# Performance work log

Measured on AMD Instinct MI355X. Metric: run time of the kernel, lower is better.

## Reference

```python
import jax, jax.numpy as jnp
import numpy as np

DT = 1e-3  # integration timestep (init kwarg dt)


def setup_inputs() -> dict:
    key = jax.random.key(0)
    ks = jax.random.split(key, 10)
    B, T, S, H = 4096, 2048, 1, 64
    # physically sensible signals: v ~ N(0,1), 0 < F_c < F_s so g > 0
    v = jax.random.normal(ks[0], (B, T, S), dtype=jnp.float32)
    F_c = 0.5 + jax.random.uniform(ks[1], (B, T, S), dtype=jnp.float32)
    F_s = F_c + 0.5 + 0.5 * jax.random.uniform(ks[2], (B, T, S), dtype=jnp.float32)
    x = jnp.concatenate([v, F_c, F_s], axis=-1)  # [B, T, 3*S]
    u01 = lambda k, shp: jax.random.uniform(k, shp, minval=0.0, maxval=0.1, dtype=jnp.float32)
    return {
        "x": x,
        "sigma_1": u01(ks[3], (1, S)),
        "sigma_2": u01(ks[4], (1, S)),
        "alpha": u01(ks[5], (1, S)),
        "v_s": u01(ks[6], (1, S)),
        "W1": jax.random.normal(ks[7], (2 * S, H), dtype=jnp.float32) * 0.1,
        "b1": jnp.zeros((H,), jnp.float32),
        "W2": jax.random.normal(ks[8], (H, S), dtype=jnp.float32) * 0.1,
        "b2": jnp.zeros((S,), jnp.float32),
    }


def reference(x, sigma_1, sigma_2, alpha, v_s, W1, b1, W2, b2):
    """LuGreCell.callv3 unrolled over time via lax.scan. x: [B,T,3S] -> F: [B,T,S]."""
    s1 = jnp.abs(sigma_1)
    s2 = jnp.abs(sigma_2)

    def step(sz0, xt):  # sz0: [B,S], xt: [B,3S]
        v, F_c, F_s = jnp.split(xt, 3, axis=-1)
        # sigma_call: MLP on concat([v, sz_0])
        mi = jnp.concatenate([v, sz0], axis=-1)  # [B, 2S]
        sigma_0 = jax.nn.softplus(jnp.tanh(mi @ W1 + b1) @ W2 + b2)  # [B, S]
        g = F_c + (F_s - F_c) * jnp.exp(-jnp.abs(v / v_s) ** alpha)
        k = g * jnp.sign(v)
        sz = k + (sz0 - k) * jnp.exp(-DT * sigma_0 * jnp.abs(v) / g)
        zdot = v - sz * jnp.abs(v) / g  # uses pre-clip sz, as in original
        sz = jnp.clip(sz, -F_s, F_s)
        F = sz + s1 * zdot + s2 * v
        return sz, F

    B = x.shape[0]
    S = x.shape[-1] // 3
    xT = jnp.swapaxes(x, 0, 1)  # [T, B, 3S]
    sz_init = jnp.zeros((B, S), x.dtype)
    _, F_seq = jax.lax.scan(step, sz_init, xT)  # F_seq: [T, B, S]
    return jnp.swapaxes(F_seq, 0, 1)  # [B, T, S]
```

## Files before the change

### kernel.cpp

```cpp
#include <hip/hip_runtime.h>


#define DT 1e-3f
#define NV 256
#define VMINF (-6.6f)
#define VMAXF (6.6f)
#define ZAF   (2.56f)

__global__ __launch_bounds__(320) void coef_nodes_kernel(
    const float* __restrict__ W1,
    const float* __restrict__ b1,
    const float* __restrict__ W2,
    const float* __restrict__ b2,
    float* __restrict__ fbuf)
{
    const int iv = blockIdx.x;
    const int j  = threadIdx.x >> 6;
    const int h  = threadIdx.x & 63;
    const float v = VMINF + iv * ((VMAXF - VMINF) / (NV - 1));
    const float pn = 0.95105651629f * ZAF;
    const float qn = 0.58778525229f * ZAF;
    const float szv = (j == 0) ? pn : (j == 1) ? -pn
                    : (j == 2) ? qn : (j == 3) ? -qn : 0.f;
    const float pre = fmaf(v, W1[h], fmaf(szv, W1[64 + h], b1[h]));
    float c = W2[h] * tanhf(pre);
#pragma unroll
    for (int o = 32; o; o >>= 1) c += __shfl_down(c, o);
    if (h == 0) {
        const float y = c + b2[0];
        fbuf[iv * 5 + j] = fmaxf(y, 0.f) + log1pf(expf(-fabsf(y)));
    }
}

__global__ __launch_bounds__(256) void lugre_kernel(
    const float* __restrict__ x,
    const float* __restrict__ sigma1,
    const float* __restrict__ sigma2,
    const float* __restrict__ alpha_p,
    const float* __restrict__ vs_p,
    const float* __restrict__ fbuf,
    float* __restrict__ out,
    int B, int T)
{
    __shared__ float4 sA[NV];
    __shared__ float  sB[NV];
    __shared__ __align__(16) float preBuf[2][16][17][12];

    {
        const int iv = threadIdx.x;
        const float f0 = fbuf[iv * 5 + 0], f1 = fbuf[iv * 5 + 1];
        const float f2 = fbuf[iv * 5 + 2], f3 = fbuf[iv * 5 + 3];
        const float f4 = fbuf[iv * 5 + 4];
        const float pn = 0.95105651629f * ZAF;
        const float qn = 0.58778525229f * ZAF;
        const float P = pn * pn, Q = qn * qn;
        const float c0 = f4;
        const float ep = 0.5f * (f0 + f1) - c0;
        const float eq = 0.5f * (f2 + f3) - c0;
        const float op = 0.5f * (f0 - f1);
        const float oq = 0.5f * (f2 - f3);
        const float invPQ = 1.f / (P - Q);
        const float c4 = (ep / P - eq / Q) * invPQ;
        const float c2 = ep / P - c4 * P;
        const float c3 = (op / pn - oq / qn) * invPQ;
        const float c1 = op / pn - c3 * P;
        sA[iv] = make_float4(-DT * c0, -DT * c1, -DT * c2, -DT * c3);
        sB[iv] = -DT * c4;
    }

    const int lane16 = threadIdx.x & 15;
    const int grp    = threadIdx.x >> 4;
    const int b      = blockIdx.x * 16 + grp;
    const int NB     = T / 16;

    const float LOG2E = 1.4426950408889634f;
    const float s1v    = fabsf(sigma1[0]);
    const float s2v    = fabsf(sigma2[0]);
    const float s12    = s1v + s2v;
    const float alpha  = alpha_p[0];
    const float inv_vs = 1.0f / vs_p[0];
    const float SVC    = (NV - 1) / (VMAXF - VMINF);
    const float VOFF   = -VMINF * SVC;
    const float IMAX   = 254.999f;

    const float* __restrict__ xb = x + (size_t)b * T * 3;
    float* __restrict__ outb = out + (size_t)b * T;

    float sz = 0.f, Fkeep = 0.f;
    float xc0, xc1, xc2, xn0, xn1, xn2;

    auto mkpre_store = [&](float v, float fc, float fs, int WB) {
        const float av = fabsf(v);
        const float u  = av * inv_vs;
        const float lg = __builtin_amdgcn_logf(u);
        const float pw = __builtin_amdgcn_exp2f(alpha * lg);
        const float w_ = __builtin_amdgcn_exp2f(-LOG2E * pw);
        const float g  = fmaf(fs - fc, w_, fc);
        const float k  = copysignf(g, v);
        const float avg = av * __builtin_amdgcn_rcpf(g);
        const float fvr = __builtin_amdgcn_fmed3f(fmaf(v, SVC, VOFF), 0.f, IMAX);
        const float fvf = floorf(fvr);
        const float fr  = fvr - fvf;
        const int   iv  = (int)fvf;
        const float4 A0 = sA[iv], A1 = sA[iv + 1];
        const float  B0 = sB[iv], B1 = sB[iv + 1];
        float* wp = &preBuf[WB][grp][lane16][0];
        *(float4*)(wp + 0) = make_float4(fmaf(fr, A1.x - A0.x, A0.x),
                                         fmaf(fr, A1.y - A0.y, A0.y),
                                         fmaf(fr, A1.z - A0.z, A0.z),
                                         fmaf(fr, A1.w - A0.w, A0.w));
        *(float4*)(wp + 4) = make_float4(fmaf(fr, B1 - B0, B0), avg, k, -(s1v * avg));
        *(float4*)(wp + 8) = make_float4(s12 * v, fs, -fs, 0.f);
    };

    auto iter = [&](int n, int RB, int WB) {
        const float* rp = &preBuf[RB][grp][0][0];
        float4 s0a = *(const float4*)(rp + 0);
        float4 s0b = *(const float4*)(rp + 4);
        float4 s0c = *(const float4*)(rp + 8);
        float4 s1a = *(const float4*)(rp + 12);
        float4 s1b = *(const float4*)(rp + 16);
        float4 s1c = *(const float4*)(rp + 20);
        const int bl = min(n + 3, NB - 1);
        const int tl = 3 * (16 * bl + lane16);
        const float f0 = xb[tl], f1 = xb[tl + 1], f2 = xb[tl + 2];
        mkpre_store(xc0, xc1, xc2, WB);

#pragma unroll
        for (int t = 0; t < 16; ++t) {
            float4 na = s1a, nb = s1b, nc = s1c;
            if (t < 14) {
                const float* q = rp + (t + 2) * 12;
                na = *(const float4*)(q + 0);
                nb = *(const float4*)(q + 4);
                nc = *(const float4*)(q + 8);
            }
            const float h   = fmaf(fmaf(fmaf(fmaf(s0b.x, sz, s0a.w), sz, s0a.z), sz, s0a.y), sz, s0a.x);
            const float xd  = h * s0b.y;
            const float dd  = fmaf(xd, fmaf(xd, 0.5f, 1.f), 1.f);
            const float szn = fmaf(dd, sz - s0b.z, s0b.z);
            const float szc = __builtin_amdgcn_fmed3f(szn, s0c.z, s0c.y);
            const float F   = fmaf(s0b.w, szn, s0c.x + szc);
            sz = szc;
            Fkeep = (lane16 == t) ? F : Fkeep;
            s0a = s1a; s0b = s1b; s0c = s1c;
            s1a = na;  s1b = nb;  s1c = nc;
        }
        outb[16 * n + lane16] = Fkeep;
        xc0 = xn0; xc1 = xn1; xc2 = xn2;
        xn0 = f0;  xn1 = f1;  xn2 = f2;
    };

    const int t0i = 3 * lane16;
    const float p0 = xb[t0i], p1 = xb[t0i + 1], p2 = xb[t0i + 2];
    const int t1i = 3 * (16 + lane16);
    xc0 = xb[t1i]; xc1 = xb[t1i + 1]; xc2 = xb[t1i + 2];
    const int t2i = 3 * (32 + lane16);
    xn0 = xb[t2i]; xn1 = xb[t2i + 1]; xn2 = xb[t2i + 2];

    __syncthreads();
    mkpre_store(p0, p1, p2, 0);

    for (int nn = 0; nn < NB; nn += 2) {
        iter(nn, 0, 1);
        iter(nn + 1, 1, 0);
    }
}

extern "C" void kernel_launch(void* const* d_in, const int* in_sizes, int n_in,
                              void* d_out, int out_size, void* d_ws, size_t ws_size,
                              hipStream_t stream) {
    const float* x  = (const float*)d_in[0];
    const float* s1 = (const float*)d_in[1];
    const float* s2 = (const float*)d_in[2];
    const float* al = (const float*)d_in[3];
    const float* vs = (const float*)d_in[4];
    const float* W1 = (const float*)d_in[5];
    const float* b1 = (const float*)d_in[6];
    const float* W2 = (const float*)d_in[7];
    const float* b2 = (const float*)d_in[8];
    float* out  = (float*)d_out;
    float* fbuf = (float*)d_ws;

    const int T = 2048;
    const int B = out_size / T;

    coef_nodes_kernel<<<NV, 320, 0, stream>>>(W1, b1, W2, b2, fbuf);
    lugre_kernel<<<B / 16, 256, 0, stream>>>(x, s1, s2, al, vs, fbuf, out, B, T);
}
```

Before: 264.8 us.

## Shorten serial recurrence chain, shrink per-step buffer, move coefficient table to global

Coefficient fitting moves into the node kernel, which writes final polynomial tables to global memory. The main kernel drops its shared-memory tables and gathers from global one block ahead. The per-step record shrinks from 12 to 8 floats by pre-multiplying the coefficients by |v|/g. The output F is now computed once per lane after the 16-step loop instead of every step. The recurrence polynomial is evaluated Estrin-style to shorten the serial dependency chain on sz, at the cost of extra registers and possibly different rounding.

```diff
diff --git a/kernel.cpp b/kernel.cpp
--- a/kernel.cpp
+++ b/kernel.cpp
@@ -7,13 +7,15 @@
 #define VMAXF (6.6f)
 #define ZAF   (2.56f)
 
-__global__ __launch_bounds__(320) void coef_nodes_kernel(
+__global__ __launch_bounds__(320) void coef_kernel(
     const float* __restrict__ W1,
     const float* __restrict__ b1,
     const float* __restrict__ W2,
     const float* __restrict__ b2,
-    float* __restrict__ fbuf)
+    float4* __restrict__ tabA,
+    float*  __restrict__ tabB)
 {
+    __shared__ float fsh[5];
     const int iv = blockIdx.x;
     const int j  = threadIdx.x >> 6;
     const int h  = threadIdx.x & 63;
@@ -28,33 +30,13 @@
     for (int o = 32; o; o >>= 1) c += __shfl_down(c, o);
     if (h == 0) {
         const float y = c + b2[0];
-        fbuf[iv * 5 + j] = fmaxf(y, 0.f) + log1pf(expf(-fabsf(y)));
+        fsh[j] = fmaxf(y, 0.f) + log1pf(expf(-fabsf(y)));
     }
-}
-
-__global__ __launch_bounds__(256) void lugre_kernel(
-    const float* __restrict__ x,
-    const float* __restrict__ sigma1,
-    const float* __restrict__ sigma2,
-    const float* __restrict__ alpha_p,
-    const float* __restrict__ vs_p,
-    const float* __restrict__ fbuf,
-    float* __restrict__ out,
-    int B, int T)
-{
-    __shared__ float4 sA[NV];
-    __shared__ float  sB[NV];
-    __shared__ __align__(16) float preBuf[2][16][17][12];
-
-    {
-        const int iv = threadIdx.x;
-        const float f0 = fbuf[iv * 5 + 0], f1 = fbuf[iv * 5 + 1];
-        const float f2 = fbuf[iv * 5 + 2], f3 = fbuf[iv * 5 + 3];
-        const float f4 = fbuf[iv * 5 + 4];
-        const float pn = 0.95105651629f * ZAF;
-        const float qn = 0.58778525229f * ZAF;
+    __syncthreads();
+    if (threadIdx.x == 0) {
+        const float f0 = fsh[0], f1 = fsh[1], f2 = fsh[2], f3 = fsh[3];
+        const float c0 = fsh[4];
         const float P = pn * pn, Q = qn * qn;
-        const float c0 = f4;
         const float ep = 0.5f * (f0 + f1) - c0;
         const float eq = 0.5f * (f2 + f3) - c0;
         const float op = 0.5f * (f0 - f1);
@@ -64,9 +46,23 @@
         const float c2 = ep / P - c4 * P;
         const float c3 = (op / pn - oq / qn) * invPQ;
         const float c1 = op / pn - c3 * P;
-        sA[iv] = make_float4(-DT * c0, -DT * c1, -DT * c2, -DT * c3);
-        sB[iv] = -DT * c4;
+        tabA[iv] = make_float4(-DT * c0, -DT * c1, -DT * c2, -DT * c3);
+        tabB[iv] = -DT * c4;
     }
+}
+
+__global__ __launch_bounds__(256) void lugre_kernel(
+    const float* __restrict__ x,
+    const float* __restrict__ sigma1,
+    const float* __restrict__ sigma2,
+    const float* __restrict__ alpha_p,
+    const float* __restrict__ vs_p,
+    const float4* __restrict__ tabA,
+    const float*  __restrict__ tabB,
+    float* __restrict__ out,
+    int B, int T)
+{
+    __shared__ __align__(16) float preBuf[2][16][17][8];
 
     const int lane16 = threadIdx.x & 15;
     const int grp    = threadIdx.x >> 4;
@@ -86,10 +82,24 @@
     const float* __restrict__ xb = x + (size_t)b * T * 3;
     float* __restrict__ outb = out + (size_t)b * T;
 
-    float sz = 0.f, Fkeep = 0.f;
+    float sz = 0.f, sznKeep = 0.f;
     float xc0, xc1, xc2, xn0, xn1, xn2;
-
-    auto mkpre_store = [&](float v, float fc, float fs, int WB) {
+    float4 gA0, gA1; float gB0, gB1, gfr;
+    float curQ, curSv, curFs, nxtQ, nxtSv, nxtFs;
+
+    auto gather = [&](float v, float4& A0, float4& A1,
+                      float& B0, float& B1, float& fr) {
+        const float fvr = __builtin_amdgcn_fmed3f(fmaf(v, SVC, VOFF), 0.f, IMAX);
+        const float fvf = floorf(fvr);
+        fr = fvr - fvf;
+        const int iv = (int)fvf;
+        A0 = tabA[iv]; A1 = tabA[iv + 1];
+        B0 = tabB[iv]; B1 = tabB[iv + 1];
+    };
+
+    auto finish = [&](float v, float fc, float fs,
+                      float4 A0, float4 A1, float B0, float B1, float fr,
+                      int WB, float& oQ, float& oSv, float& oFs) {
         const float av = fabsf(v);
         const float u  = av * inv_vs;
         const float lg = __builtin_amdgcn_logf(u);
@@ -98,57 +108,59 @@
         const float g  = fmaf(fs - fc, w_, fc);
         const float k  = copysignf(g, v);
         const float avg = av * __builtin_amdgcn_rcpf(g);
-        const float fvr = __builtin_amdgcn_fmed3f(fmaf(v, SVC, VOFF), 0.f, IMAX);
-        const float fvf = floorf(fvr);
-        const float fr  = fvr - fvf;
-        const int   iv  = (int)fvf;
-        const float4 A0 = sA[iv], A1 = sA[iv + 1];
-        const float  B0 = sB[iv], B1 = sB[iv + 1];
+        const float e0m = fmaf(fr, A1.x - A0.x, A0.x) * avg;
+        const float e1m = fmaf(fr, A1.y - A0.y, A0.y) * avg;
+        const float e2m = fmaf(fr, A1.z - A0.z, A0.z) * avg;
+        const float e3m = fmaf(fr, A1.w - A0.w, A0.w) * avg;
+        const float e4m = fmaf(fr, B1 - B0, B0) * avg;
         float* wp = &preBuf[WB][grp][lane16][0];
-        *(float4*)(wp + 0) = make_float4(fmaf(fr, A1.x - A0.x, A0.x),
-                                         fmaf(fr, A1.y - A0.y, A0.y),
-                                         fmaf(fr, A1.z - A0.z, A0.z),
-                                         fmaf(fr, A1.w - A0.w, A0.w));
-        *(float4*)(wp + 4) = make_float4(fmaf(fr, B1 - B0, B0), avg, k, -(s1v * avg));
-        *(float4*)(wp + 8) = make_float4(s12 * v, fs, -fs, 0.f);
+        ((float4*)wp)[0] = make_float4(e0m, e1m, e2m, e3m);
+        ((float4*)wp)[1] = make_float4(e4m, k, fs, 0.f);
+        oQ  = -(s1v * avg);
+        oSv = s12 * v;
+        oFs = fs;
     };
 
     auto iter = [&](int n, int RB, int WB) {
-        const float* rp = &preBuf[RB][grp][0][0];
-        float4 s0a = *(const float4*)(rp + 0);
-        float4 s0b = *(const float4*)(rp + 4);
-        float4 s0c = *(const float4*)(rp + 8);
-        float4 s1a = *(const float4*)(rp + 12);
-        float4 s1b = *(const float4*)(rp + 16);
-        float4 s1c = *(const float4*)(rp + 20);
+        const float4* rp = (const float4*)&preBuf[RB][grp][0][0];
+        float4 s0a = rp[0], s0b = rp[1];
+        float4 s1a = rp[2], s1b = rp[3];
         const int bl = min(n + 3, NB - 1);
         const int tl = 3 * (16 * bl + lane16);
         const float f0 = xb[tl], f1 = xb[tl + 1], f2 = xb[tl + 2];
-        mkpre_store(xc0, xc1, xc2, WB);
+        float4 nA0, nA1; float nB0, nB1, nfr;
+        gather(xn0, nA0, nA1, nB0, nB1, nfr);
+        finish(xc0, xc1, xc2, gA0, gA1, gB0, gB1, gfr, WB, nxtQ, nxtSv, nxtFs);
 
 #pragma unroll
         for (int t = 0; t < 16; ++t) {
-            float4 na = s1a, nb = s1b, nc = s1c;
+            float4 na = s1a, nb = s1b;
             if (t < 14) {
-                const float* q = rp + (t + 2) * 12;
-                na = *(const float4*)(q + 0);
-                nb = *(const float4*)(q + 4);
-                nc = *(const float4*)(q + 8);
+                na = rp[2 * (t + 2)];
+                nb = rp[2 * (t + 2) + 1];
             }
-            const float h   = fmaf(fmaf(fmaf(fmaf(s0b.x, sz, s0a.w), sz, s0a.z), sz, s0a.y), sz, s0a.x);
-            const float xd  = h * s0b.y;
-            const float dd  = fmaf(xd, fmaf(xd, 0.5f, 1.f), 1.f);
-            const float szn = fmaf(dd, sz - s0b.z, s0b.z);
-            const float szc = __builtin_amdgcn_fmed3f(szn, s0c.z, s0c.y);
-            const float F   = fmaf(s0b.w, szn, s0c.x + szc);
+            const float t1  = fmaf(s0a.y, sz, s0a.x);
+            const float t2  = fmaf(s0a.w, sz, s0a.z);
+            const float z2  = sz * sz;
+            const float smk = sz - s0b.y;
+            const float t12 = fmaf(t2, z2, t1);
+            const float z4  = z2 * z2;
+            const float xd  = fmaf(s0b.x, z4, t12);
+            const float u_  = fmaf(xd, 0.5f, 1.f);
+            const float w_  = xd * u_;
+            const float szn = fmaf(smk, w_, sz);
+            const float szc = __builtin_amdgcn_fmed3f(szn, -s0b.z, s0b.z);
             sz = szc;
-            Fkeep = (lane16 == t) ? F : Fkeep;
-            s0a = s1a; s0b = s1b; s0c = s1c;
-            s1a = na;  s1b = nb;  s1c = nc;
+            sznKeep = (lane16 == t) ? szn : sznKeep;
+            s0a = s1a; s0b = s1b; s1a = na; s1b = nb;
         }
-        outb[16 * n + lane16] = Fkeep;
+        const float szcK = __builtin_amdgcn_fmed3f(sznKeep, -curFs, curFs);
+        const float F    = fmaf(curQ, sznKeep, curSv + szcK);
+        outb[16 * n + lane16] = F;
         xc0 = xn0; xc1 = xn1; xc2 = xn2;
         xn0 = f0;  xn1 = f1;  xn2 = f2;
+        gA0 = nA0; gA1 = nA1; gB0 = nB0; gB1 = nB1; gfr = nfr;
+        curQ = nxtQ; curSv = nxtSv; curFs = nxtFs;
     };
 
     const int t0i = 3 * lane16;
@@ -158,8 +170,10 @@
     const int t2i = 3 * (32 + lane16);
     xn0 = xb[t2i]; xn1 = xb[t2i + 1]; xn2 = xb[t2i + 2];
 
-    __syncthreads();
-    mkpre_store(p0, p1, p2, 0);
+    float4 aA0, aA1; float aB0, aB1, afr;
+    gather(p0, aA0, aA1, aB0, aB1, afr);
+    finish(p0, p1, p2, aA0, aA1, aB0, aB1, afr, 0, curQ, curSv, curFs);
+    gather(xc0, gA0, gA1, gB0, gB1, gfr);
 
     for (int nn = 0; nn < NB; nn += 2) {
         iter(nn, 0, 1);
@@ -179,12 +193,15 @@
     const float* b1 = (const float*)d_in[6];
     const float* W2 = (const float*)d_in[7];
     const float* b2 = (const float*)d_in[8];
-    float* out  = (float*)d_out;
-    float* fbuf = (float*)d_ws;
+    float* out = (float*)d_out;
+
+    float4* tabA = (float4*)d_ws;
+    float*  tabB = (float*)((char*)d_ws + NV * 16);
 
     const int T = 2048;
     const int B = out_size / T;
 
-    coef_nodes_kernel<<<NV, 320, 0, stream>>>(W1, b1, W2, b2, fbuf);
-    lugre_kernel<<<B / 16, 256, 0, stream>>>(x, s1, s2, al, vs, fbuf, out, B, T);
+    coef_kernel<<<NV, 320, 0, stream>>>(W1, b1, W2, b2, tabA, tabB);
+    lugre_kernel<<<B / 16, 256, 0, stream>>>(x, s1, s2, al, vs, tabA, tabB,
+                                             out, B, T);
 }
```

Result: slower. 284.1 us (+7.3%).
